# Performance work log

Measured on AMD Instinct MI355X. Metric: run time of the kernel, lower is better.

The kernel has to match this reference:

```python
import jax, jax.numpy as jnp
import numpy as np

D_MODEL = 1024
NUM_HEADS = 16
D_K = D_MODEL // NUM_HEADS


def setup_inputs() -> dict:
    key = jax.random.key(0)
    ks = jax.random.split(key, 11)
    B, S = 2, 2048
    scale = 1.0 / np.sqrt(D_MODEL)
    inp = {
        'q': jax.random.normal(ks[0], (B, S, D_MODEL), dtype=jnp.float32),
        'k': jax.random.normal(ks[1], (B, S, D_MODEL), dtype=jnp.float32),
        'v': jax.random.normal(ks[2], (B, S, D_MODEL), dtype=jnp.float32),
        'W_q': jax.random.normal(ks[3], (D_MODEL, D_MODEL), dtype=jnp.float32) * scale,
        'b_q': jnp.zeros((D_MODEL,), dtype=jnp.float32),
        'W_k': jax.random.normal(ks[4], (D_MODEL, D_MODEL), dtype=jnp.float32) * scale,
        'b_k': jnp.zeros((D_MODEL,), dtype=jnp.float32),
        'W_v': jax.random.normal(ks[5], (D_MODEL, D_MODEL), dtype=jnp.float32) * scale,
        'b_v': jnp.zeros((D_MODEL,), dtype=jnp.float32),
        'W_o': jax.random.normal(ks[6], (D_MODEL, D_MODEL), dtype=jnp.float32) * scale,
        'b_o': jnp.zeros((D_MODEL,), dtype=jnp.float32),
    }
    return inp


def _split_heads(x):
    # [B, S, D] -> [B, H, S, d_k]
    B, S, _ = x.shape
    return x.reshape(B, S, NUM_HEADS, D_K).transpose(0, 2, 1, 3)


def reference(q, k, v, W_q, b_q, W_k, b_k, W_v, b_v, W_o, b_o):
    # Linear projections (torch Linear: x @ W.T + b)
    qh = _split_heads(q @ W_q.T + b_q)  # [B,H,S,dk]
    kh = _split_heads(k @ W_k.T + b_k)
    vh = _split_heads(v @ W_v.T + b_v)
    scores = jnp.einsum('bhsd,bhtd->bhst', qh, kh) / jnp.sqrt(
        jnp.asarray(D_K, dtype=qh.dtype))  # [B,H,S,S]
    probs = jax.nn.softmax(scores, axis=-1)
    attn = jnp.einsum('bhst,bhtd->bhsd', probs, vh)  # [B,H,S,dk]
    B, H, S, dk = attn.shape
    combined = attn.transpose(0, 2, 1, 3).reshape(B, S, H * dk)  # [B,S,D]
    return combined @ W_o.T + b_o
```

## Files before the change

kernel.cpp:

```cpp
#include <hip/hip_runtime.h>
#include <hip/hip_bf16.h>

typedef __bf16 bf16;
typedef __attribute__((ext_vector_type(4))) __bf16 bf16x4;
typedef __attribute__((ext_vector_type(8))) __bf16 bf16x8;
typedef __attribute__((ext_vector_type(4))) float f32x4;

#define AS1C(p) ((const __attribute__((address_space(1))) void*)(p))
#define AS3(p)  ((__attribute__((address_space(3))) void*)(p))

static constexpr int B_ = 2, S_ = 2048, DM = 1024, H_ = 16, DK = 64;
static constexpr int M_ = B_ * S_;
static constexpr int NW = DM * DM;
static constexpr float QSCL = 0.125f * 1.44269504088896340736f;

__device__ __forceinline__ float fast_exp2(float x) {
#if __has_builtin(__builtin_amdgcn_exp2f)
  return __builtin_amdgcn_exp2f(x);
#else
  return exp2f(x);
#endif
}

__global__ __launch_bounds__(256) void cast_w3(
    const float* Wq, const float* Wk, const float* Wv, bf16* outw)
{
  const int z = blockIdx.y;
  const float* in = z == 0 ? Wq : (z == 1 ? Wk : Wv);
  const float s = z == 0 ? QSCL : 1.0f;
  bf16* out = outw + (size_t)z * NW;
  const int i = (blockIdx.x * 256 + threadIdx.x) * 8;
  f32x4 a = *(const f32x4*)(in + i);
  f32x4 b = *(const f32x4*)(in + i + 4);
  bf16x8 o;
#pragma unroll
  for (int j = 0; j < 4; ++j) { o[j] = (bf16)(a[j] * s); o[4 + j] = (bf16)(b[j] * s); }
  *(bf16x8*)(out + i) = o;
}

__global__ __launch_bounds__(256) void cast_f32_bf16(
    const float* __restrict__ in, bf16* __restrict__ out)
{
  const int i = (blockIdx.x * 256 + threadIdx.x) * 8;
  f32x4 a = *(const f32x4*)(in + i);
  f32x4 b = *(const f32x4*)(in + i + 4);
  bf16x8 o;
#pragma unroll
  for (int j = 0; j < 4; ++j) { o[j] = (bf16)a[j]; o[4 + j] = (bf16)b[j]; }
  *(bf16x8*)(out + i) = o;
}

template<int WTM, bool A_BF16, bool OUT_F32>
__device__ __forceinline__ void gemm_body(
    const void* __restrict__ Ain, const bf16* __restrict__ W,
    const float* __restrict__ bias, float bscale, void* __restrict__ Cout,
    bool transv, int M, int N, int K, int bx, int by)
{
  constexpr int BMt = 2 * WTM;
  constexpr int WI  = WTM / 16;
  __shared__ bf16 As[2 * BMt * 32];
  __shared__ bf16 Bs[2 * 128 * 32];

  const int tid  = threadIdx.x;
  const int wave = tid >> 6, lane = tid & 63;
  const int quad = lane >> 4, l16 = lane & 15;
  const int wm = wave >> 1, wn = wave & 1;
  const int row0 = by * BMt;
  const int col0 = bx * 128;

  const int srow  = lane >> 2;
  const int skcol = (lane & 3) * 8;

  const int arow  = tid >> 1;
  const int ak16  = (tid & 1) * 16;
  const float* agp = nullptr;
  f32x4 pre[8];
  if constexpr (!A_BF16) {
    agp = (const float*)Ain + (size_t)(row0 + arow) * K + ak16;
#pragma unroll
    for (int hf = 0; hf < 2; ++hf)
#pragma unroll
      for (int c = 0; c < 4; ++c)
        pre[hf * 4 + c] = *(const f32x4*)(agp + hf * 32 + c * 4);
  }

  f32x4 acc[WI][4] = {};

  for (int k0 = 0; k0 < K; k0 += 64) {
    __syncthreads();
    if constexpr (A_BF16) {
      const bf16* A = (const bf16*)Ain;
#pragma unroll
      for (int hf = 0; hf < 2; ++hf)
#pragma unroll
        for (int c = wave; c < BMt / 16; c += 4)
          __builtin_amdgcn_global_load_lds(
              AS1C(A + (size_t)(row0 + c * 16 + srow) * K + k0 + hf * 32 + skcol),
              AS3(As + hf * BMt * 32 + c * 16 * 32), 16, 0, 0);
    } else {
#pragma unroll
      for (int hf = 0; hf < 2; ++hf) {
        bf16x8 w0, w1;
#pragma unroll
        for (int j = 0; j < 4; ++j) {
          w0[j]     = (bf16)pre[hf * 4 + 0][j];
          w0[4 + j] = (bf16)pre[hf * 4 + 1][j];
          w1[j]     = (bf16)pre[hf * 4 + 2][j];
          w1[4 + j] = (bf16)pre[hf * 4 + 3][j];
        }
        bf16* dst = As + hf * BMt * 32 + arow * 32 + ak16;
        *(bf16x8*)dst = w0;
        *(bf16x8*)(dst + 8) = w1;
      }
    }
#pragma unroll
    for (int hf = 0; hf < 2; ++hf)
#pragma unroll
      for (int i = 0; i < 2; ++i) {
        const int c = wave * 2 + i;
        __builtin_amdgcn_global_load_lds(
            AS1C(W + (size_t)(col0 + c * 16 + srow) * K + k0 + hf * 32 + skcol),
            AS3(Bs + hf * 128 * 32 + c * 16 * 32), 16, 0, 0);
      }
    __syncthreads();

    if constexpr (!A_BF16) {
      if (k0 + 64 < K) {
#pragma unroll
        for (int hf = 0; hf < 2; ++hf)
#pragma unroll
          for (int c = 0; c < 4; ++c)
            pre[hf * 4 + c] = *(const f32x4*)(agp + k0 + 64 + hf * 32 + c * 4);
      }
    }

#pragma unroll
    for (int hf = 0; hf < 2; ++hf) {
      bf16x8 a[WI], bfr[4];
#pragma unroll
      for (int i = 0; i < WI; ++i)
        a[i] = *(const bf16x8*)(As + hf * BMt * 32 + (wm * WTM + i * 16 + l16) * 32 + quad * 8);
#pragma unroll
      for (int j = 0; j < 4; ++j)
        bfr[j] = *(const bf16x8*)(Bs + hf * 128 * 32 + (wn * 64 + j * 16 + l16) * 32 + quad * 8);
#pragma unroll
      for (int i = 0; i < WI; ++i)
#pragma unroll
        for (int j = 0; j < 4; ++j)
          acc[i][j] = __builtin_amdgcn_mfma_f32_16x16x32_bf16(a[i], bfr[j], acc[i][j], 0, 0, 0);
    }
  }

#pragma unroll
  for (int j = 0; j < 4; ++j) {
    const int col = col0 + wn * 64 + j * 16 + l16;
    const float bv = bias[col] * bscale;
    if (!OUT_F32 && transv) {
      const int hh = col >> 6, dd = col & 63;
#pragma unroll
      for (int i = 0; i < WI; ++i) {
        const int row = row0 + wm * WTM + i * 16 + quad * 4;
        const int bb2 = row >> 11, tok = row & 2047;
        bf16x4 o;
#pragma unroll
        for (int r = 0; r < 4; ++r) o[r] = (bf16)(acc[i][j][r] + bv);
        *(bf16x4*)((bf16*)Cout + (((size_t)bb2 * H_ + hh) * DK + dd) * S_ + tok) = o;
      }
    } else {
#pragma unroll
      for (int i = 0; i < WI; ++i) {
#pragma unroll
        for (int r = 0; r < 4; ++r) {
          const int row = row0 + wm * WTM + i * 16 + quad * 4 + r;
          const float val = acc[i][j][r] + bv;
          if constexpr (OUT_F32)
            ((float*)Cout)[(size_t)row * N + col] = val;
          else
            ((bf16*)Cout)[(size_t)row * N + col] = (bf16)val;
        }
      }
    }
  }
}

template<int WTM, bool A_BF16, bool OUT_F32>
__global__ __launch_bounds__(256) void gemm_bt(
    const void* __restrict__ Ain, const bf16* __restrict__ W,
    const float* __restrict__ bias, void* __restrict__ Cout,
    int M, int N, int K)
{
  gemm_body<WTM, A_BF16, OUT_F32>(Ain, W, bias, 1.0f, Cout, false, M, N, K,
                                  blockIdx.x, blockIdx.y);
}

__global__ __launch_bounds__(256) void gemm_qkv(
    const float* A0, const float* A1, const float* A2,
    const bf16* __restrict__ Wc,
    const float* b0, const float* b1, const float* b2,
    bf16* C0, bf16* C1, bf16* C2, int M, int N, int K)
{
  const int z = blockIdx.z;
  const float* A = z == 0 ? A0 : (z == 1 ? A1 : A2);
  const float* bias = z == 0 ? b0 : (z == 1 ? b1 : b2);
  const float bscale = z == 0 ? QSCL : 1.0f;
  bf16* C = z == 0 ? C0 : (z == 1 ? C1 : C2);
  gemm_body<64, false, false>(A, Wc + (size_t)z * NW, bias, bscale, C,
                              z == 2, M, N, K, blockIdx.x, blockIdx.y);
}

__global__ __launch_bounds__(256, 3) void attn_kernel(
    const bf16* __restrict__ Q, const bf16* __restrict__ Kb,
    const bf16* __restrict__ Vtg, bf16* __restrict__ O)
{
  __shared__ bf16 Kt[2][64 * 72];
  __shared__ bf16 Vt[2][64 * 72];
  __shared__ bf16 Ps[4 * 16 * 72];

  const int tid  = threadIdx.x;
  const int wave = tid >> 6, lane = tid & 63;
  const int quad = lane >> 4, l16 = lane & 15;
  const int b = blockIdx.z, h = blockIdx.y;
  const int q0 = blockIdx.x * 64 + wave * 16;
  const size_t base  = (size_t)b * S_ * DM + (size_t)h * DK;
  const size_t baseV = ((size_t)b * H_ + h) * DK * S_;

  bf16x8 qf[2];
#pragma unroll
  for (int kt = 0; kt < 2; ++kt)
    qf[kt] = *(const bf16x8*)(Q + base + (size_t)(q0 + l16) * DM + kt * 32 + quad * 8);

  const bool kside = (wave < 2);
  const int srow  = kside ? (tid >> 1) : ((tid - 128) >> 1);
  const int shalf = tid & 1;
  const bf16* gp = kside
      ? (Kb + base + (size_t)srow * DM + shalf * 32)
      : (Vtg + baseV + (size_t)srow * S_ + shalf * 32);
  const size_t gstep = kside ? (size_t)64 * DM : 64;
  bf16* ldst0 = (kside ? Kt[0] : Vt[0]) + srow * 72 + shalf * 32;
  bf16* ldst1 = (kside ? Kt[1] : Vt[1]) + srow * 72 + shalf * 32;

  bf16x8 st[4];
#pragma unroll
  for (int c = 0; c < 4; ++c) st[c] = *(const bf16x8*)(gp + c * 8);
#pragma unroll
  for (int c = 0; c < 4; ++c) *(bf16x8*)(ldst0 + c * 8) = st[c];
  gp += gstep;
#pragma unroll
  for (int c = 0; c < 4; ++c) st[c] = *(const bf16x8*)(gp + c * 8);
  gp += gstep;

  f32x4 lacc = {0.f, 0.f, 0.f, 0.f};
  f32x4 accO[4] = {};
  bf16* Pw = Ps + wave * 16 * 72;

  constexpr int NIT = S_ / 64;
  for (int it = 0; it < NIT; ++it) {
    const int bsel = it & 1;
    __syncthreads();

    if (it + 1 < NIT) {
      bf16* dst = bsel ? ldst0 : ldst1;
#pragma unroll
      for (int c = 0; c < 4; ++c) *(bf16x8*)(dst + c * 8) = st[c];
      if (it + 2 < NIT) {
#pragma unroll
        for (int c = 0; c < 4; ++c) st[c] = *(const bf16x8*)(gp + c * 8);
        gp += gstep;
      }
    }

    const bf16* Kc = Kt[bsel];
    const bf16* Vc = Vt[bsel];

    f32x4 sc[4];
#pragma unroll
    for (int ct = 0; ct < 4; ++ct) {
      const bf16* kp = Kc + (ct * 16 + l16) * 72 + quad * 8;
      f32x4 a = {0.f, 0.f, 0.f, 0.f};
      a = __builtin_amdgcn_mfma_f32_16x16x32_bf16(*(const bf16x8*)kp,        qf[0], a, 0, 0, 0);
      a = __builtin_amdgcn_mfma_f32_16x16x32_bf16(*(const bf16x8*)(kp + 32), qf[1], a, 0, 0, 0);
      sc[ct] = a;
    }

#pragma unroll
    for (int ct = 0; ct < 4; ++ct) {
      bf16x4 pk;
#pragma unroll
      for (int r = 0; r < 4; ++r) {
        const float p = fast_exp2(sc[ct][r]);
        lacc[r] += p;
        pk[r] = (bf16)p;
      }
      *(bf16x4*)(Pw + l16 * 72 + ct * 16 + quad * 4) = pk;
    }
    bf16x8 pf0 = *(const bf16x8*)(Pw + l16 * 72 + quad * 8);
    bf16x8 pf1 = *(const bf16x8*)(Pw + l16 * 72 + 32 + quad * 8);

#pragma unroll
    for (int dt = 0; dt < 4; ++dt) {
      const bf16* vp = Vc + (dt * 16 + l16) * 72;
      accO[dt] = __builtin_amdgcn_mfma_f32_16x16x32_bf16(
          *(const bf16x8*)(vp + quad * 8),      pf0, accO[dt], 0, 0, 0);
      accO[dt] = __builtin_amdgcn_mfma_f32_16x16x32_bf16(
          *(const bf16x8*)(vp + 32 + quad * 8), pf1, accO[dt], 0, 0, 0);
    }
  }

  float l_s = (lacc[0] + lacc[1]) + (lacc[2] + lacc[3]);
  l_s += __shfl_xor(l_s, 16, 64);
  l_s += __shfl_xor(l_s, 32, 64);
  const float inv = 1.0f / l_s;
#pragma unroll
  for (int dt = 0; dt < 4; ++dt) {
    bf16x4 o;
#pragma unroll
    for (int r = 0; r < 4; ++r) o[r] = (bf16)(accO[dt][r] * inv);
    *(bf16x4*)(O + base + (size_t)(q0 + l16) * DM + dt * 16 + quad * 4) = o;
  }
}

extern "C" void kernel_launch(void* const* d_in, const int* in_sizes, int n_in,
                              void* d_out, int out_size, void* d_ws, size_t ws_size,
                              hipStream_t stream) {
  (void)in_sizes; (void)n_in; (void)out_size; (void)ws_size;
  const float* q  = (const float*)d_in[0];
  const float* k  = (const float*)d_in[1];
  const float* v  = (const float*)d_in[2];
  const float* Wq = (const float*)d_in[3];
  const float* bq = (const float*)d_in[4];
  const float* Wk = (const float*)d_in[5];
  const float* bk = (const float*)d_in[6];
  const float* Wv = (const float*)d_in[7];
  const float* bvv= (const float*)d_in[8];
  const float* Wo = (const float*)d_in[9];
  const float* bo = (const float*)d_in[10];
  float* out = (float*)d_out;

  char* ws = (char*)d_ws;
  const size_t MB = 1024 * 1024;
  bf16* Qb  = (bf16*)(ws);
  bf16* Kbf = (bf16*)(ws + 8 * MB);
  bf16* Vtg = (bf16*)(ws + 16 * MB);
  bf16* Wc  = (bf16*)(ws + 24 * MB);
  bf16* Ab  = (bf16*)(ws + 24 * MB);
  bf16* WoC = (bf16*)(ws + 8 * MB);

  dim3 bb(256, 1, 1);

  cast_w3<<<dim3(NW / 2048, 3, 1), bb, 0, stream>>>(Wq, Wk, Wv, Wc);

  gemm_qkv<<<dim3(DM / 128, M_ / 128, 3), bb, 0, stream>>>(
      q, k, v, Wc, bq, bk, bvv, Qb, Kbf, Vtg, M_, DM, DM);

  attn_kernel<<<dim3(S_ / 64, H_, B_), bb, 0, stream>>>(Qb, Kbf, Vtg, Ab);

  cast_f32_bf16<<<dim3(NW / 2048, 1, 1), bb, 0, stream>>>(Wo, WoC);

  gemm_bt<32, true, true><<<dim3(DM / 128, M_ / 64, 1), bb, 0, stream>>>(
      Ab, WoC, bo, out, M_, DM, DM);
}
```

Before: 251.8 us.

## Widen attention tile to 32 rows per wave, merge weight casts, remap grids

The attention kernel now gives each wave two 16-row query fragments, 128 queries per block. Each K/V fragment loaded from LDS therefore feeds twice as many MFMAs. It drops LDS double buffering for a single buffer with two barriers per iteration, and removes the occupancy hint from launch bounds. The Wo cast is folded into the QKV weight cast kernel, and all grids become 1D with a block-index remap that groups blocks by row tile or head. Attention output is written in place over Q, the workspace layout changes, and the A-row index is masked to the tile height. The single-buffer K/V staging and extra barrier may expose load latency, and higher register use may cut occupancy.

Result: faster. 223.2 us (-11.4%).

```diff
diff --git a/kernel.cpp b/kernel.cpp
--- a/kernel.cpp
+++ b/kernel.cpp
@@ -22,31 +22,20 @@
 #endif
 }
 
-__global__ __launch_bounds__(256) void cast_w3(
-    const float* Wq, const float* Wk, const float* Wv, bf16* outw)
+__global__ __launch_bounds__(256) void cast_w4(
+    const float* Wq, const float* Wk, const float* Wv, const float* Wo,
+    bf16* Wc, bf16* WoC)
 {
   const int z = blockIdx.y;
-  const float* in = z == 0 ? Wq : (z == 1 ? Wk : Wv);
+  const float* in = z == 0 ? Wq : (z == 1 ? Wk : (z == 2 ? Wv : Wo));
   const float s = z == 0 ? QSCL : 1.0f;
-  bf16* out = outw + (size_t)z * NW;
+  bf16* out = z < 3 ? (Wc + (size_t)z * NW) : WoC;
   const int i = (blockIdx.x * 256 + threadIdx.x) * 8;
   f32x4 a = *(const f32x4*)(in + i);
   f32x4 b = *(const f32x4*)(in + i + 4);
   bf16x8 o;
 #pragma unroll
   for (int j = 0; j < 4; ++j) { o[j] = (bf16)(a[j] * s); o[4 + j] = (bf16)(b[j] * s); }
-  *(bf16x8*)(out + i) = o;
-}
-
-__global__ __launch_bounds__(256) void cast_f32_bf16(
-    const float* __restrict__ in, bf16* __restrict__ out)
-{
-  const int i = (blockIdx.x * 256 + threadIdx.x) * 8;
-  f32x4 a = *(const f32x4*)(in + i);
-  f32x4 b = *(const f32x4*)(in + i + 4);
-  bf16x8 o;
-#pragma unroll
-  for (int j = 0; j < 4; ++j) { o[j] = (bf16)a[j]; o[4 + j] = (bf16)b[j]; }
   *(bf16x8*)(out + i) = o;
 }
 
@@ -71,7 +60,7 @@
   const int srow  = lane >> 2;
   const int skcol = (lane & 3) * 8;
 
-  const int arow  = tid >> 1;
+  const int arow  = (tid >> 1) & (BMt - 1);
   const int ak16  = (tid & 1) * 16;
   const float* agp = nullptr;
   f32x4 pre[8];
@@ -183,51 +172,61 @@
   }
 }
 
-template<int WTM, bool A_BF16, bool OUT_F32>
-__global__ __launch_bounds__(256) void gemm_bt(
-    const void* __restrict__ Ain, const bf16* __restrict__ W,
-    const float* __restrict__ bias, void* __restrict__ Cout,
-    int M, int N, int K)
-{
-  gemm_body<WTM, A_BF16, OUT_F32>(Ain, W, bias, 1.0f, Cout, false, M, N, K,
-                                  blockIdx.x, blockIdx.y);
-}
-
 __global__ __launch_bounds__(256) void gemm_qkv(
     const float* A0, const float* A1, const float* A2,
     const bf16* __restrict__ Wc,
     const float* b0, const float* b1, const float* b2,
     bf16* C0, bf16* C1, bf16* C2, int M, int N, int K)
 {
-  const int z = blockIdx.z;
+  const int id = blockIdx.x;
+  const int z  = id >> 8;
+  const int r  = id & 255;
+  const int by = r & 31;
+  const int bx = r >> 5;
   const float* A = z == 0 ? A0 : (z == 1 ? A1 : A2);
   const float* bias = z == 0 ? b0 : (z == 1 ? b1 : b2);
   const float bscale = z == 0 ? QSCL : 1.0f;
   bf16* C = z == 0 ? C0 : (z == 1 ? C1 : C2);
   gemm_body<64, false, false>(A, Wc + (size_t)z * NW, bias, bscale, C,
-                              z == 2, M, N, K, blockIdx.x, blockIdx.y);
-}
-
-__global__ __launch_bounds__(256, 3) void attn_kernel(
-    const bf16* __restrict__ Q, const bf16* __restrict__ Kb,
-    const bf16* __restrict__ Vtg, bf16* __restrict__ O)
-{
-  __shared__ bf16 Kt[2][64 * 72];
-  __shared__ bf16 Vt[2][64 * 72];
-  __shared__ bf16 Ps[4 * 16 * 72];
+                              z == 2, M, N, K, bx, by);
+}
+
+__global__ __launch_bounds__(256) void gemm_out(
+    const bf16* __restrict__ Ain, const bf16* __restrict__ W,
+    const float* __restrict__ bias, float* __restrict__ Cout,
+    int M, int N, int K)
+{
+  const int id = blockIdx.x;
+  const int by = id & 63;
+  const int bx = id >> 6;
+  gemm_body<32, true, true>(Ain, W, bias, 1.0f, Cout, false, M, N, K, bx, by);
+}
+
+__global__ __launch_bounds__(256) void attn_kernel(
+    const bf16* Q, const bf16* __restrict__ Kb,
+    const bf16* __restrict__ Vtg, bf16* O)
+{
+  __shared__ bf16 Kt[64 * 72];
+  __shared__ bf16 Vt[64 * 72];
+  __shared__ bf16 Ps[4 * 32 * 72];
 
   const int tid  = threadIdx.x;
   const int wave = tid >> 6, lane = tid & 63;
   const int quad = lane >> 4, l16 = lane & 15;
-  const int b = blockIdx.z, h = blockIdx.y;
-  const int q0 = blockIdx.x * 64 + wave * 16;
+  const int id = blockIdx.x;
+  const int hb = id & 31;
+  const int h = hb & 15, b = hb >> 4;
+  const int qt = id >> 5;
+  const int qA = qt * 128 + wave * 32;
   const size_t base  = (size_t)b * S_ * DM + (size_t)h * DK;
   const size_t baseV = ((size_t)b * H_ + h) * DK * S_;
 
-  bf16x8 qf[2];
-#pragma unroll
-  for (int kt = 0; kt < 2; ++kt)
-    qf[kt] = *(const bf16x8*)(Q + base + (size_t)(q0 + l16) * DM + kt * 32 + quad * 8);
+  bf16x8 qf[2][2];
+#pragma unroll
+  for (int f = 0; f < 2; ++f)
+#pragma unroll
+    for (int kt = 0; kt < 2; ++kt)
+      qf[f][kt] = *(const bf16x8*)(Q + base + (size_t)(qA + f * 16 + l16) * DM + kt * 32 + quad * 8);
 
   const bool kside = (wave < 2);
   const int srow  = kside ? (tid >> 1) : ((tid - 128) >> 1);
@@ -236,86 +235,92 @@
       ? (Kb + base + (size_t)srow * DM + shalf * 32)
       : (Vtg + baseV + (size_t)srow * S_ + shalf * 32);
   const size_t gstep = kside ? (size_t)64 * DM : 64;
-  bf16* ldst0 = (kside ? Kt[0] : Vt[0]) + srow * 72 + shalf * 32;
-  bf16* ldst1 = (kside ? Kt[1] : Vt[1]) + srow * 72 + shalf * 32;
+  bf16* ldst = (kside ? Kt : Vt) + srow * 72 + shalf * 32;
 
   bf16x8 st[4];
-#pragma unroll
-  for (int c = 0; c < 4; ++c) st[c] = *(const bf16x8*)(gp + c * 8);
-#pragma unroll
-  for (int c = 0; c < 4; ++c) *(bf16x8*)(ldst0 + c * 8) = st[c];
-  gp += gstep;
 #pragma unroll
   for (int c = 0; c < 4; ++c) st[c] = *(const bf16x8*)(gp + c * 8);
   gp += gstep;
 
-  f32x4 lacc = {0.f, 0.f, 0.f, 0.f};
-  f32x4 accO[4] = {};
-  bf16* Pw = Ps + wave * 16 * 72;
+  f32x4 lacc[2] = {};
+  f32x4 accO[2][4] = {};
+  bf16* Pw = Ps + wave * 32 * 72;
 
   constexpr int NIT = S_ / 64;
   for (int it = 0; it < NIT; ++it) {
-    const int bsel = it & 1;
     __syncthreads();
+#pragma unroll
+    for (int c = 0; c < 4; ++c) *(bf16x8*)(ldst + c * 8) = st[c];
+    __syncthreads();
 
     if (it + 1 < NIT) {
-      bf16* dst = bsel ? ldst0 : ldst1;
-#pragma unroll
-      for (int c = 0; c < 4; ++c) *(bf16x8*)(dst + c * 8) = st[c];
-      if (it + 2 < NIT) {
-#pragma unroll
-        for (int c = 0; c < 4; ++c) st[c] = *(const bf16x8*)(gp + c * 8);
-        gp += gstep;
-      }
-    }
-
-    const bf16* Kc = Kt[bsel];
-    const bf16* Vc = Vt[bsel];
-
-    f32x4 sc[4];
+#pragma unroll
+      for (int c = 0; c < 4; ++c) st[c] = *(const bf16x8*)(gp + c * 8);
+      gp += gstep;
+    }
+
+    f32x4 sc[2][4];
 #pragma unroll
     for (int ct = 0; ct < 4; ++ct) {
-      const bf16* kp = Kc + (ct * 16 + l16) * 72 + quad * 8;
-      f32x4 a = {0.f, 0.f, 0.f, 0.f};
-      a = __builtin_amdgcn_mfma_f32_16x16x32_bf16(*(const bf16x8*)kp,        qf[0], a, 0, 0, 0);
-      a = __builtin_amdgcn_mfma_f32_16x16x32_bf16(*(const bf16x8*)(kp + 32), qf[1], a, 0, 0, 0);
-      sc[ct] = a;
-    }
-
-#pragma unroll
-    for (int ct = 0; ct < 4; ++ct) {
-      bf16x4 pk;
-#pragma unroll
-      for (int r = 0; r < 4; ++r) {
-        const float p = fast_exp2(sc[ct][r]);
-        lacc[r] += p;
-        pk[r] = (bf16)p;
-      }
-      *(bf16x4*)(Pw + l16 * 72 + ct * 16 + quad * 4) = pk;
-    }
-    bf16x8 pf0 = *(const bf16x8*)(Pw + l16 * 72 + quad * 8);
-    bf16x8 pf1 = *(const bf16x8*)(Pw + l16 * 72 + 32 + quad * 8);
+      const bf16* kp = Kt + (ct * 16 + l16) * 72 + quad * 8;
+      const bf16x8 kf0 = *(const bf16x8*)kp;
+      const bf16x8 kf1 = *(const bf16x8*)(kp + 32);
+#pragma unroll
+      for (int f = 0; f < 2; ++f) {
+        f32x4 a = {0.f, 0.f, 0.f, 0.f};
+        a = __builtin_amdgcn_mfma_f32_16x16x32_bf16(kf0, qf[f][0], a, 0, 0, 0);
+        a = __builtin_amdgcn_mfma_f32_16x16x32_bf16(kf1, qf[f][1], a, 0, 0, 0);
+        sc[f][ct] = a;
+      }
+    }
+
+#pragma unroll
+    for (int f = 0; f < 2; ++f)
+#pragma unroll
+      for (int ct = 0; ct < 4; ++ct) {
+        bf16x4 pk;
+#pragma unroll
+        for (int r = 0; r < 4; ++r) {
+          const float p = fast_exp2(sc[f][ct][r]);
+          lacc[f][r] += p;
+          pk[r] = (bf16)p;
+        }
+        *(bf16x4*)(Pw + (f * 16 + l16) * 72 + ct * 16 + quad * 4) = pk;
+      }
+
+    bf16x8 pf[2][2];
+#pragma unroll
+    for (int f = 0; f < 2; ++f) {
+      pf[f][0] = *(const bf16x8*)(Pw + (f * 16 + l16) * 72 + quad * 8);
+      pf[f][1] = *(const bf16x8*)(Pw + (f * 16 + l16) * 72 + 32 + quad * 8);
+    }
 
 #pragma unroll
     for (int dt = 0; dt < 4; ++dt) {
-      const bf16* vp = Vc + (dt * 16 + l16) * 72;
-      accO[dt] = __builtin_amdgcn_mfma_f32_16x16x32_bf16(
-          *(const bf16x8*)(vp + quad * 8),      pf0, accO[dt], 0, 0, 0);
-      accO[dt] = __builtin_amdgcn_mfma_f32_16x16x32_bf16(
-          *(const bf16x8*)(vp + 32 + quad * 8), pf1, accO[dt], 0, 0, 0);
-    }
-  }
-
-  float l_s = (lacc[0] + lacc[1]) + (lacc[2] + lacc[3]);
-  l_s += __shfl_xor(l_s, 16, 64);
-  l_s += __shfl_xor(l_s, 32, 64);
-  const float inv = 1.0f / l_s;
-#pragma unroll
-  for (int dt = 0; dt < 4; ++dt) {
-    bf16x4 o;
-#pragma unroll
-    for (int r = 0; r < 4; ++r) o[r] = (bf16)(accO[dt][r] * inv);
-    *(bf16x4*)(O + base + (size_t)(q0 + l16) * DM + dt * 16 + quad * 4) = o;
+      const bf16* vp = Vt + (dt * 16 + l16) * 72;
+      const bf16x8 vf0 = *(const bf16x8*)(vp + quad * 8);
+      const bf16x8 vf1 = *(const bf16x8*)(vp + 32 + quad * 8);
+#pragma unroll
+      for (int f = 0; f < 2; ++f) {
+        accO[f][dt] = __builtin_amdgcn_mfma_f32_16x16x32_bf16(vf0, pf[f][0], accO[f][dt], 0, 0, 0);
+        accO[f][dt] = __builtin_amdgcn_mfma_f32_16x16x32_bf16(vf1, pf[f][1], accO[f][dt], 0, 0, 0);
+      }
+    }
+  }
+
+#pragma unroll
+  for (int f = 0; f < 2; ++f) {
+    float l_s = (lacc[f][0] + lacc[f][1]) + (lacc[f][2] + lacc[f][3]);
+    l_s += __shfl_xor(l_s, 16, 64);
+    l_s += __shfl_xor(l_s, 32, 64);
+    const float inv = 1.0f / l_s;
+#pragma unroll
+    for (int dt = 0; dt < 4; ++dt) {
+      bf16x4 o;
+#pragma unroll
+      for (int r = 0; r < 4; ++r) o[r] = (bf16)(accO[f][dt][r] * inv);
+      *(bf16x4*)(O + base + (size_t)(qA + f * 16 + l16) * DM + dt * 16 + quad * 4) = o;
+    }
   }
 }
 
@@ -342,20 +347,17 @@
   bf16* Kbf = (bf16*)(ws + 8 * MB);
   bf16* Vtg = (bf16*)(ws + 16 * MB);
   bf16* Wc  = (bf16*)(ws + 24 * MB);
-  bf16* Ab  = (bf16*)(ws + 24 * MB);
-  bf16* WoC = (bf16*)(ws + 8 * MB);
+  bf16* WoC = (bf16*)(ws + 30 * MB);
+  bf16* Ab  = Qb;
 
   dim3 bb(256, 1, 1);
 
-  cast_w3<<<dim3(NW / 2048, 3, 1), bb, 0, stream>>>(Wq, Wk, Wv, Wc);
-
-  gemm_qkv<<<dim3(DM / 128, M_ / 128, 3), bb, 0, stream>>>(
+  cast_w4<<<dim3(NW / 2048, 4, 1), bb, 0, stream>>>(Wq, Wk, Wv, Wo, Wc, WoC);
+
+  gemm_qkv<<<dim3(768, 1, 1), bb, 0, stream>>>(
       q, k, v, Wc, bq, bk, bvv, Qb, Kbf, Vtg, M_, DM, DM);
 
-  attn_kernel<<<dim3(S_ / 64, H_, B_), bb, 0, stream>>>(Qb, Kbf, Vtg, Ab);
-
-  cast_f32_bf16<<<dim3(NW / 2048, 1, 1), bb, 0, stream>>>(Wo, WoC);
-
-  gemm_bt<32, true, true><<<dim3(DM / 128, M_ / 64, 1), bb, 0, stream>>>(
-      Ab, WoC, bo, out, M_, DM, DM);
-}
+  attn_kernel<<<dim3(512, 1, 1), bb, 0, stream>>>(Qb, Kbf, Vtg, Ab);
+
+  gemm_out<<<dim3(512, 1, 1), bb, 0, stream>>>(Ab, WoC, bo, out, M_, DM, DM);
+}
```
